# Performance work log

Measured on AMD Instinct MI355X. Metric: run time of the kernel, lower is better.

Reference implementation:

```python
import jax, jax.numpy as jnp
import numpy as np

B, T, I, H, P = 256, 2048, 2, 128, 129  # batch, max_len, input feats, hidden, num_pitches


def setup_inputs() -> dict:
    key = jax.random.key(0)
    ks = jax.random.split(key, 8)
    s = 1.0 / np.sqrt(H)  # torch LSTM/Linear init scale
    x = jax.random.normal(ks[0], (B, T, I), jnp.float32)
    lengths = jax.random.randint(ks[1], (B,), 1, T + 1, jnp.int32)
    W_ih = jax.random.uniform(ks[2], (4 * H, I), jnp.float32, -s, s)
    W_hh = jax.random.uniform(ks[3], (4 * H, H), jnp.float32, -s, s)
    note_W = jax.random.uniform(ks[4], (P, H), jnp.float32, -s, s)
    note_b = jax.random.uniform(ks[5], (P,), jnp.float32, -s, s)
    dur_W = jax.random.uniform(ks[6], (1, H), jnp.float32, -s, s)
    dur_b = jax.random.uniform(ks[7], (1,), jnp.float32, -s, s)
    return dict(x=x, lengths=lengths, W_ih=W_ih, W_hh=W_hh,
                note_W=note_W, note_b=note_b, dur_W=dur_W, dur_b=dur_b)


def _lstm(x, lengths, W_ih, W_hh):
    # Precompute input projections for all timesteps in one GEMM: [T,B,4H]
    pre = jnp.einsum('bti,gi->tbg', x, W_ih)
    h0 = jnp.zeros((x.shape[0], W_hh.shape[1]), x.dtype)
    c0 = h0
    ts = jnp.arange(x.shape[1])

    def step(carry, inp):
        h, c = carry
        px, t = inp
        gates = px + h @ W_hh.T  # [B,4H], torch gate order: i,f,g,o
        i_g, f_g, g_g, o_g = jnp.split(gates, 4, axis=-1)
        i_g = jax.nn.sigmoid(i_g)
        f_g = jax.nn.sigmoid(f_g)
        o_g = jax.nn.sigmoid(o_g)
        g_g = jnp.tanh(g_g)
        c_new = f_g * c + i_g * g_g
        h_new = o_g * jnp.tanh(c_new)
        m = (t < lengths)[:, None]  # packed semantics: freeze past length
        h2 = jnp.where(m, h_new, h)
        c2 = jnp.where(m, c_new, c)
        return (h2, c2), jnp.where(m, h_new, 0.0)

    (hT, cT), hs = jax.lax.scan(step, (h0, c0), (pre, ts))
    return jnp.transpose(hs, (1, 0, 2)), hT, cT  # [B,T,H], final states = states at last valid step


def reference(x, lengths, W_ih, W_hh, note_W, note_b, dur_W, dur_b):
    hs, hT, cT = _lstm(x, lengths, W_ih, W_hh)
    mask = (jnp.arange(x.shape[1])[None, :] < lengths[:, None])[..., None]
    note_logits = jnp.where(mask, hs @ note_W.T + note_b, 0.0)     # [B,T,129]
    duration_pred = jnp.where(mask, hs @ dur_W.T + dur_b, 0.0)     # [B,T,1]
    return note_logits, duration_pred, hT, cT
```

## Files before the change

kernel.cpp:

```cpp
#include <hip/hip_runtime.h>


typedef _Float16 f16;
typedef _Float16 f16x2 __attribute__((ext_vector_type(2)));
typedef _Float16 f16x8 __attribute__((ext_vector_type(8)));
typedef float    f32x4 __attribute__((ext_vector_type(4)));

#define B_  256
#define T_  2048
#define H_  128
#define P_  129

static constexpr size_t NOTE_N   = (size_t)B_ * T_ * P_;
static constexpr size_t DUR_BASE = NOTE_N;
static constexpr size_t HT_BASE  = DUR_BASE + (size_t)B_ * T_;
static constexpr size_t CT_BASE  = HT_BASE + (size_t)B_ * H_;

#if defined(__has_builtin)
#if __has_builtin(__builtin_amdgcn_fdot2)
#define HAVE_FDOT2 1
#endif
#if __has_builtin(__builtin_amdgcn_exp2f)
#define EXP2F(x) __builtin_amdgcn_exp2f(x)
#endif
#endif
#ifndef EXP2F
#define EXP2F(x) __expf((x) * 0.6931471805599453f)
#endif

__device__ __forceinline__ float dot2_acc(f16x2 a, f16x2 b, float c) {
#ifdef HAVE_FDOT2
    return __builtin_amdgcn_fdot2(a, b, c, false);
#else
    return c + (float)a[0] * (float)b[0] + (float)a[1] * (float)b[1];
#endif
}

__device__ __forceinline__ float fast_rcp(float x) { return __builtin_amdgcn_rcpf(x); }

__device__ __forceinline__ float sigmoid_f(float x) {
    float e = EXP2F(-1.44269504f * x);
    return fast_rcp(1.f + e);
}
__device__ __forceinline__ float tanh_f(float x) {
    float e = EXP2F(2.885390082f * x);
    return (e - 1.f) * fast_rcp(e + 1.f);
}

__device__ __forceinline__ float pair_allsum(float v) {
    int a = __float_as_int(v);
    v += __int_as_float(__builtin_amdgcn_mov_dpp(a, 0xB1, 0xF, 0xF, true));
    return v;
}

__device__ __forceinline__ f16* hs_row(float* out, int bt) {
    size_t byteoff = ((size_t)bt * (P_ * 4) + 15) & ~(size_t)15;
    return (f16*)((char*)out + byteoff);
}

__global__ __launch_bounds__(256) void prep_k(const float* __restrict__ note_W,
                                              const float* __restrict__ dur_W,
                                              f16* __restrict__ Wn) {
    int i = threadIdx.x + blockIdx.x * 256;
    if (i >= 144 * 128) return;
    int row = i >> 7, k = i & 127;
    float v = 0.f;
    if (row < 129)       v = note_W[row * 128 + k];
    else if (row == 129) v = dur_W[k];
    Wn[i] = (f16)v;
}

__global__ __launch_bounds__(256, 1) void lstm6_k(const float* __restrict__ x,
                                                  const int* __restrict__ lengths,
                                                  const float* __restrict__ W_ih,
                                                  const float* __restrict__ W_hh,
                                                  float* __restrict__ out) {
    __shared__ __align__(16) f16 h_sh[2][H_];
    __shared__ __align__(8) float2 xs[128];

    const int tid = threadIdx.x;
    const int b = blockIdx.x;
    const int j  = tid >> 1;
    const int kh = tid & 1;
    const bool writer = (kh == 0);

    union WU { f16x8 v8[32]; f16x2 v2[128]; } wu;
    float wix[4], wiy[4];
#pragma unroll
    for (int g = 0; g < 4; g++) {
        const int c = j + 128 * g;
        const float* wr = W_hh + (size_t)c * H_ + 64 * kh;
#pragma unroll
        for (int i = 0; i < 8; i++) {
            float4 v1 = *(const float4*)(wr + 8 * i);
            float4 v2 = *(const float4*)(wr + 8 * i + 4);
            f16x8 f;
            f[0] = (f16)v1.x; f[1] = (f16)v1.y; f[2] = (f16)v1.z; f[3] = (f16)v1.w;
            f[4] = (f16)v2.x; f[5] = (f16)v2.y; f[6] = (f16)v2.z; f[7] = (f16)v2.w;
            wu.v8[8 * g + i] = f;
        }
        wix[g] = W_ih[2 * c];
        wiy[g] = W_ih[2 * c + 1];
    }
    const int len = lengths[b];
    ((f16*)h_sh)[tid] = (f16)0.f;

    char* hp = (char*)out + (size_t)b * (T_ * 516ULL) + 2 * j;

    float c_reg = 0.f, h_reg = 0.f;

    for (int t = 0; t < len; t++) {
        if ((t & 127) == 0) {
            __syncthreads();
            if (tid < 128)
                xs[tid] = *(const float2*)(x + (size_t)b * T_ * 2 + (size_t)(t + tid) * 2);
            __syncthreads();
        }
        const int cur = t & 1;

        union HU { f16x8 v8[8]; f16x2 v2[32]; } hu;
#pragma unroll
        for (int i = 0; i < 8; i++)
            hu.v8[i] = *(const f16x8*)(&h_sh[cur][64 * kh + 8 * i]);

        float a0 = 0.f, a1 = 0.f, a2 = 0.f, a3 = 0.f;
        float b0 = 0.f, b1 = 0.f, b2 = 0.f, b3 = 0.f;
#pragma unroll
        for (int i = 0; i < 16; i++) {
            f16x2 hp0 = hu.v2[i];
            f16x2 hq0 = hu.v2[i + 16];
            a0 = dot2_acc(wu.v2[i],       hp0, a0);
            b0 = dot2_acc(wu.v2[i + 16],  hq0, b0);
            a1 = dot2_acc(wu.v2[i + 32],  hp0, a1);
            b1 = dot2_acc(wu.v2[i + 48],  hq0, b1);
            a2 = dot2_acc(wu.v2[i + 64],  hp0, a2);
            b2 = dot2_acc(wu.v2[i + 80],  hq0, b2);
            a3 = dot2_acc(wu.v2[i + 96],  hp0, a3);
            b3 = dot2_acc(wu.v2[i + 112], hq0, b3);
        }
        a0 += b0; a1 += b1; a2 += b2; a3 += b3;
        a0 = pair_allsum(a0);
        a1 = pair_allsum(a1);
        a2 = pair_allsum(a2);
        a3 = pair_allsum(a3);
        const float2 xv = xs[t & 127];
        a0 += __builtin_fmaf(wiy[0], xv.y, wix[0] * xv.x);
        a1 += __builtin_fmaf(wiy[1], xv.y, wix[1] * xv.x);
        a2 += __builtin_fmaf(wiy[2], xv.y, wix[2] * xv.x);
        a3 += __builtin_fmaf(wiy[3], xv.y, wix[3] * xv.x);

        const float ig = sigmoid_f(a0);
        const float fg = sigmoid_f(a1);
        const float gg = tanh_f(a2);
        const float og = sigmoid_f(a3);
        c_reg = __builtin_fmaf(fg, c_reg, ig * gg);
        h_reg = og * tanh_f(fminf(fmaxf(c_reg, -15.f), 15.f));

        if (writer) {
            const f16 h16 = (f16)h_reg;
            *(f16*)hp = h16;
            h_sh[cur ^ 1][j] = h16;
        }
        hp += 512 + (((t & 3) == 0) ? 16 : 0);

        asm volatile("s_waitcnt lgkmcnt(0)" ::: "memory");
        __builtin_amdgcn_sched_barrier(0);
        __builtin_amdgcn_s_barrier();
        __builtin_amdgcn_sched_barrier(0);
    }

    if (writer) {
        out[HT_BASE + (size_t)b * H_ + j] = h_reg;
        out[CT_BASE + (size_t)b * H_ + j] = c_reg;
    }
}

__global__ __launch_bounds__(256) void proj_k(const int* __restrict__ lengths,
                                              const f16* __restrict__ Wn,
                                              const float* __restrict__ note_b,
                                              const float* __restrict__ dur_b,
                                              float* __restrict__ out) {
    __shared__ __align__(16) f16 wn_sh[144 * 136];

    const int tid = threadIdx.x;
    {
        unsigned int* dst = (unsigned int*)wn_sh;
        const unsigned int* src = (const unsigned int*)Wn;
        for (int w = tid; w < 144 * 64; w += 256) {
            int row = w >> 6, cw = w & 63;
            dst[row * 68 + cw] = src[w];
        }
    }
    __syncthreads();

    const int wv = tid >> 6;
    const int l = tid & 63;
    const int tile = blockIdx.x * 4 + wv;
    const int bt0 = tile * 16;
    const int b = bt0 >> 11;
    const int t0 = bt0 & 2047;
    const int len = lengths[b];
    const int r16 = l & 15, q = l >> 4;

    f32x4 acc[9];
#pragma unroll
    for (int nf = 0; nf < 9; nf++) acc[nf] = f32x4{0.f, 0.f, 0.f, 0.f};

    const bool live = (t0 < len);
    if (live) {
        f16x8 a[4];
        {
            const f16* ar = hs_row(out, bt0 + r16);
#pragma unroll
            for (int kk = 0; kk < 4; kk++)
                a[kk] = *(const f16x8*)(ar + kk * 32 + q * 8);
        }
#pragma unroll
        for (int nf = 0; nf < 9; nf++) {
            const f16* brow = wn_sh + (nf * 16 + r16) * 136 + q * 8;
#pragma unroll
            for (int kk = 0; kk < 4; kk++) {
                f16x8 bb = *(const f16x8*)(brow + kk * 32);
                acc[nf] = __builtin_amdgcn_mfma_f32_16x16x32_f16(a[kk], bb, acc[nf], 0, 0, 0);
            }
        }
    }

#pragma unroll
    for (int nf = 0; nf < 9; nf++) {
        int col = nf * 16 + r16;
        float bias = 0.f;
        if (col < 129)       bias = note_b[col];
        else if (col == 129) bias = dur_b[0];
#pragma unroll
        for (int r = 0; r < 4; r++) {
            int rowbt = bt0 + q * 4 + r;
            int t = t0 + q * 4 + r;
            float v = (t < len) ? (acc[nf][r] + bias) : 0.f;
            if (col < 129)
                out[(size_t)rowbt * P_ + col] = v;
            else if (col == 129)
                out[DUR_BASE + rowbt] = v;
        }
    }
}

extern "C" void kernel_launch(void* const* d_in, const int* in_sizes, int n_in,
                              void* d_out, int out_size, void* d_ws, size_t ws_size,
                              hipStream_t stream) {
    const float* x       = (const float*)d_in[0];
    const int*   lengths = (const int*)d_in[1];
    const float* W_ih    = (const float*)d_in[2];
    const float* W_hh    = (const float*)d_in[3];
    const float* note_W  = (const float*)d_in[4];
    const float* note_b  = (const float*)d_in[5];
    const float* dur_W   = (const float*)d_in[6];
    const float* dur_b   = (const float*)d_in[7];
    float* out = (float*)d_out;
    f16* Wn = (f16*)d_ws;

    prep_k<<<72, 256, 0, stream>>>(note_W, dur_W, Wn);
    lstm6_k<<<B_, 256, 0, stream>>>(x, lengths, W_ih, W_hh, out);
    proj_k<<<(B_ * T_) / 64, 256, 0, stream>>>(lengths, Wn, note_b, dur_b, out);
}
```

Baseline: 1.127 ms.

## Pack two batch rows per block, one on MFMA and one on dot2 units

The LSTM kernel now runs two sequences per 512-thread block. The first half computes the recurrent matvec with 16x16x32 f16 MFMA instructions and the second half keeps the dot2 path, so matrix and vector units work at the same time. Both halves share the per-step block barrier and loop to the longer of the two lengths, masking updates past each sequence's own length. This halves the block count to 128 on a device with more CUs, at the cost of lockstep coupling and wasted steps on the shorter sequence. The MFMA path also wastes three quarters of its output lanes.

```diff
diff --git a/kernel.cpp b/kernel.cpp
--- a/kernel.cpp
+++ b/kernel.cpp
@@ -57,6 +57,12 @@
     size_t byteoff = ((size_t)bt * (P_ * 4) + 15) & ~(size_t)15;
     return (f16*)((char*)out + byteoff);
 }
+
+#define STEP_BARRIER()                                         \
+    asm volatile("s_waitcnt lgkmcnt(0)" ::: "memory");         \
+    __builtin_amdgcn_sched_barrier(0);                         \
+    __builtin_amdgcn_s_barrier();                              \
+    __builtin_amdgcn_sched_barrier(0);
 
 __global__ __launch_bounds__(256) void prep_k(const float* __restrict__ note_W,
                                               const float* __restrict__ dur_W,
@@ -70,108 +76,208 @@
     Wn[i] = (f16)v;
 }
 
-__global__ __launch_bounds__(256, 1) void lstm6_k(const float* __restrict__ x,
-                                                  const int* __restrict__ lengths,
-                                                  const float* __restrict__ W_ih,
-                                                  const float* __restrict__ W_hh,
-                                                  float* __restrict__ out) {
-    __shared__ __align__(16) f16 h_sh[2][H_];
-    __shared__ __align__(8) float2 xs[128];
+__global__ __launch_bounds__(512, 2) void lstm10_k(const float* __restrict__ x,
+                                                   const int* __restrict__ lengths,
+                                                   const float* __restrict__ W_ih,
+                                                   const float* __restrict__ W_hh,
+                                                   float* __restrict__ out) {
+    __shared__ __align__(16) f16 h_shA[2][H_];
+    __shared__ __align__(16) f16 h_shB[2][H_];
+    __shared__ __align__(8) float2 xsA[128];
+    __shared__ __align__(8) float2 xsB[128];
 
     const int tid = threadIdx.x;
-    const int b = blockIdx.x;
-    const int j  = tid >> 1;
-    const int kh = tid & 1;
-    const bool writer = (kh == 0);
-
-    union WU { f16x8 v8[32]; f16x2 v2[128]; } wu;
-    float wix[4], wiy[4];
-#pragma unroll
-    for (int g = 0; g < 4; g++) {
-        const int c = j + 128 * g;
-        const float* wr = W_hh + (size_t)c * H_ + 64 * kh;
-#pragma unroll
-        for (int i = 0; i < 8; i++) {
-            float4 v1 = *(const float4*)(wr + 8 * i);
-            float4 v2 = *(const float4*)(wr + 8 * i + 4);
-            f16x8 f;
-            f[0] = (f16)v1.x; f[1] = (f16)v1.y; f[2] = (f16)v1.z; f[3] = (f16)v1.w;
-            f[4] = (f16)v2.x; f[5] = (f16)v2.y; f[6] = (f16)v2.z; f[7] = (f16)v2.w;
-            wu.v8[8 * g + i] = f;
-        }
-        wix[g] = W_ih[2 * c];
-        wiy[g] = W_ih[2 * c + 1];
-    }
-    const int len = lengths[b];
-    ((f16*)h_sh)[tid] = (f16)0.f;
-
-    char* hp = (char*)out + (size_t)b * (T_ * 516ULL) + 2 * j;
-
-    float c_reg = 0.f, h_reg = 0.f;
-
-    for (int t = 0; t < len; t++) {
-        if ((t & 127) == 0) {
-            __syncthreads();
-            if (tid < 128)
-                xs[tid] = *(const float2*)(x + (size_t)b * T_ * 2 + (size_t)(t + tid) * 2);
-            __syncthreads();
-        }
-        const int cur = t & 1;
-
-        union HU { f16x8 v8[8]; f16x2 v2[32]; } hu;
-#pragma unroll
-        for (int i = 0; i < 8; i++)
-            hu.v8[i] = *(const f16x8*)(&h_sh[cur][64 * kh + 8 * i]);
-
-        float a0 = 0.f, a1 = 0.f, a2 = 0.f, a3 = 0.f;
-        float b0 = 0.f, b1 = 0.f, b2 = 0.f, b3 = 0.f;
-#pragma unroll
-        for (int i = 0; i < 16; i++) {
-            f16x2 hp0 = hu.v2[i];
-            f16x2 hq0 = hu.v2[i + 16];
-            a0 = dot2_acc(wu.v2[i],       hp0, a0);
-            b0 = dot2_acc(wu.v2[i + 16],  hq0, b0);
-            a1 = dot2_acc(wu.v2[i + 32],  hp0, a1);
-            b1 = dot2_acc(wu.v2[i + 48],  hq0, b1);
-            a2 = dot2_acc(wu.v2[i + 64],  hp0, a2);
-            b2 = dot2_acc(wu.v2[i + 80],  hq0, b2);
-            a3 = dot2_acc(wu.v2[i + 96],  hp0, a3);
-            b3 = dot2_acc(wu.v2[i + 112], hq0, b3);
-        }
-        a0 += b0; a1 += b1; a2 += b2; a3 += b3;
-        a0 = pair_allsum(a0);
-        a1 = pair_allsum(a1);
-        a2 = pair_allsum(a2);
-        a3 = pair_allsum(a3);
-        const float2 xv = xs[t & 127];
-        a0 += __builtin_fmaf(wiy[0], xv.y, wix[0] * xv.x);
-        a1 += __builtin_fmaf(wiy[1], xv.y, wix[1] * xv.x);
-        a2 += __builtin_fmaf(wiy[2], xv.y, wix[2] * xv.x);
-        a3 += __builtin_fmaf(wiy[3], xv.y, wix[3] * xv.x);
-
-        const float ig = sigmoid_f(a0);
-        const float fg = sigmoid_f(a1);
-        const float gg = tanh_f(a2);
-        const float og = sigmoid_f(a3);
-        c_reg = __builtin_fmaf(fg, c_reg, ig * gg);
-        h_reg = og * tanh_f(fminf(fmaxf(c_reg, -15.f), 15.f));
+    const int g = blockIdx.x;
+    const int bA = 2 * g, bB = 2 * g + 1;
+    const int lenA = lengths[bA], lenB = lengths[bB];
+    const int maxlen = max(lenA, lenB);
+
+    if (tid < 256) ((f16*)h_shA)[tid] = (f16)0.f;
+    else           ((f16*)h_shB)[tid - 256] = (f16)0.f;
+
+    if (tid < 256) {
+        const int w = tid >> 6, l = tid & 63;
+        const int p = l & 15, q = l >> 4;
+        const int sel = q >> 1;
+        const int j = 16 * w + 64 * sel + p;
+        const bool writer = ((q & 1) == 0);
+
+        f16x8 Bf[8][4];
+        float wxx[8], wxy[8];
+#pragma unroll
+        for (int s = 0; s < 8; s++) {
+            const int c = 16 * (w + 4 * s) + p;
+            const float* wr = W_hh + (size_t)c * H_ + 8 * q;
+#pragma unroll
+            for (int kt = 0; kt < 4; kt++) {
+                float4 v1 = *(const float4*)(wr + 32 * kt);
+                float4 v2 = *(const float4*)(wr + 32 * kt + 4);
+                f16x8 f;
+                f[0]=(f16)v1.x; f[1]=(f16)v1.y; f[2]=(f16)v1.z; f[3]=(f16)v1.w;
+                f[4]=(f16)v2.x; f[5]=(f16)v2.y; f[6]=(f16)v2.z; f[7]=(f16)v2.w;
+                Bf[s][kt] = f;
+            }
+            wxx[s] = W_ih[2 * c];
+            wxy[s] = W_ih[2 * c + 1];
+        }
+
+        char* hp = (char*)out + (size_t)bA * (T_ * 516ULL) + 2 * j;
+        const f32x4 z4 = {0.f, 0.f, 0.f, 0.f};
+        float c_reg = 0.f, h_reg = 0.f;
+
+        for (int t = 0; t < maxlen; t++) {
+            if ((t & 127) == 0) {
+                __syncthreads();
+                if (tid < 128)
+                    xsA[tid] = *(const float2*)(x + (size_t)bA * T_ * 2 + (size_t)(t + tid) * 2);
+                __syncthreads();
+            }
+            const int cur = t & 1;
+
+            f16x8 Af[4];
+#pragma unroll
+            for (int kt = 0; kt < 4; kt++)
+                Af[kt] = *(const f16x8*)(&h_shA[cur][32 * kt + 8 * q]);
+
+            f32x4 acc[8];
+#pragma unroll
+            for (int s = 0; s < 8; s++)
+                acc[s] = __builtin_amdgcn_mfma_f32_16x16x32_f16(Af[0], Bf[s][0], z4, 0, 0, 0);
+#pragma unroll
+            for (int kt = 1; kt < 4; kt++) {
+#pragma unroll
+                for (int s = 0; s < 8; s++)
+                    acc[s] = __builtin_amdgcn_mfma_f32_16x16x32_f16(
+                        Af[kt], Bf[s][kt], acc[s], 0, 0, 0);
+            }
+
+            const float2 xv = xsA[t & 127];
+            float G[4];
+#pragma unroll
+            for (int tt = 0; tt < 4; tt++) {
+                float ga = acc[2 * tt][0] +
+                           __builtin_fmaf(wxy[2 * tt], xv.y, wxx[2 * tt] * xv.x);
+                float gb = acc[2 * tt + 1][0] +
+                           __builtin_fmaf(wxy[2 * tt + 1], xv.y, wxx[2 * tt + 1] * xv.x);
+                G[tt] = sel ? gb : ga;
+            }
+
+            const float ig = sigmoid_f(G[0]);
+            const float fg = sigmoid_f(G[1]);
+            const float gg = tanh_f(G[2]);
+            const float og = sigmoid_f(G[3]);
+            float cn = __builtin_fmaf(fg, c_reg, ig * gg);
+            float hn = og * tanh_f(fminf(fmaxf(cn, -15.f), 15.f));
+            const bool m = (t < lenA);
+            c_reg = m ? cn : c_reg;
+            h_reg = m ? hn : h_reg;
+
+            if (writer) {
+                const f16 h16 = (f16)h_reg;
+                if (m) *(f16*)hp = h16;
+                h_shA[cur ^ 1][j] = h16;
+            }
+            hp += 512 + (((t & 3) == 0) ? 16 : 0);
+
+            STEP_BARRIER();
+        }
 
         if (writer) {
-            const f16 h16 = (f16)h_reg;
-            *(f16*)hp = h16;
-            h_sh[cur ^ 1][j] = h16;
-        }
-        hp += 512 + (((t & 3) == 0) ? 16 : 0);
-
-        asm volatile("s_waitcnt lgkmcnt(0)" ::: "memory");
-        __builtin_amdgcn_sched_barrier(0);
-        __builtin_amdgcn_s_barrier();
-        __builtin_amdgcn_sched_barrier(0);
-    }
-
-    if (writer) {
-        out[HT_BASE + (size_t)b * H_ + j] = h_reg;
-        out[CT_BASE + (size_t)b * H_ + j] = c_reg;
+            out[HT_BASE + (size_t)bA * H_ + j] = h_reg;
+            out[CT_BASE + (size_t)bA * H_ + j] = c_reg;
+        }
+    } else {
+        const int ltid = tid - 256;
+        const int j = ltid >> 1;
+        const int kh = ltid & 1;
+        const bool writer = (kh == 0);
+
+        union WU { f16x8 v8[32]; f16x2 v2[128]; } wu;
+        float wix[4], wiy[4];
+#pragma unroll
+        for (int gg_ = 0; gg_ < 4; gg_++) {
+            const int c = j + 128 * gg_;
+            const float* wr = W_hh + (size_t)c * H_ + 64 * kh;
+#pragma unroll
+            for (int i = 0; i < 8; i++) {
+                float4 v1 = *(const float4*)(wr + 8 * i);
+                float4 v2 = *(const float4*)(wr + 8 * i + 4);
+                f16x8 f;
+                f[0]=(f16)v1.x; f[1]=(f16)v1.y; f[2]=(f16)v1.z; f[3]=(f16)v1.w;
+                f[4]=(f16)v2.x; f[5]=(f16)v2.y; f[6]=(f16)v2.z; f[7]=(f16)v2.w;
+                wu.v8[8 * gg_ + i] = f;
+            }
+            wix[gg_] = W_ih[2 * c];
+            wiy[gg_] = W_ih[2 * c + 1];
+        }
+
+        char* hp = (char*)out + (size_t)bB * (T_ * 516ULL) + 2 * j;
+        float c_reg = 0.f, h_reg = 0.f;
+
+        for (int t = 0; t < maxlen; t++) {
+            if ((t & 127) == 0) {
+                __syncthreads();
+                if (ltid < 128)
+                    xsB[ltid] = *(const float2*)(x + (size_t)bB * T_ * 2 + (size_t)(t + ltid) * 2);
+                __syncthreads();
+            }
+            const int cur = t & 1;
+
+            union HU { f16x8 v8[8]; f16x2 v2[32]; } hu;
+#pragma unroll
+            for (int i = 0; i < 8; i++)
+                hu.v8[i] = *(const f16x8*)(&h_shB[cur][64 * kh + 8 * i]);
+
+            float a0 = 0.f, a1 = 0.f, a2 = 0.f, a3 = 0.f;
+            float b0 = 0.f, b1 = 0.f, b2 = 0.f, b3 = 0.f;
+#pragma unroll
+            for (int i = 0; i < 16; i++) {
+                f16x2 hp0 = hu.v2[i];
+                f16x2 hq0 = hu.v2[i + 16];
+                a0 = dot2_acc(wu.v2[i],       hp0, a0);
+                b0 = dot2_acc(wu.v2[i + 16],  hq0, b0);
+                a1 = dot2_acc(wu.v2[i + 32],  hp0, a1);
+                b1 = dot2_acc(wu.v2[i + 48],  hq0, b1);
+                a2 = dot2_acc(wu.v2[i + 64],  hp0, a2);
+                b2 = dot2_acc(wu.v2[i + 80],  hq0, b2);
+                a3 = dot2_acc(wu.v2[i + 96],  hp0, a3);
+                b3 = dot2_acc(wu.v2[i + 112], hq0, b3);
+            }
+            a0 += b0; a1 += b1; a2 += b2; a3 += b3;
+            a0 = pair_allsum(a0);
+            a1 = pair_allsum(a1);
+            a2 = pair_allsum(a2);
+            a3 = pair_allsum(a3);
+            const float2 xv = xsB[t & 127];
+            a0 += __builtin_fmaf(wiy[0], xv.y, wix[0] * xv.x);
+            a1 += __builtin_fmaf(wiy[1], xv.y, wix[1] * xv.x);
+            a2 += __builtin_fmaf(wiy[2], xv.y, wix[2] * xv.x);
+            a3 += __builtin_fmaf(wiy[3], xv.y, wix[3] * xv.x);
+
+            const float ig = sigmoid_f(a0);
+            const float fg = sigmoid_f(a1);
+            const float gg = tanh_f(a2);
+            const float og = sigmoid_f(a3);
+            float cn = __builtin_fmaf(fg, c_reg, ig * gg);
+            float hn = og * tanh_f(fminf(fmaxf(cn, -15.f), 15.f));
+            const bool m = (t < lenB);
+            c_reg = m ? cn : c_reg;
+            h_reg = m ? hn : h_reg;
+
+            if (writer) {
+                const f16 h16 = (f16)h_reg;
+                if (m) *(f16*)hp = h16;
+                h_shB[cur ^ 1][j] = h16;
+            }
+            hp += 512 + (((t & 3) == 0) ? 16 : 0);
+
+            STEP_BARRIER();
+        }
+
+        if (writer) {
+            out[HT_BASE + (size_t)bB * H_ + j] = h_reg;
+            out[CT_BASE + (size_t)bB * H_ + j] = c_reg;
+        }
     }
 }
 
@@ -260,6 +366,6 @@
     f16* Wn = (f16*)d_ws;
 
     prep_k<<<72, 256, 0, stream>>>(note_W, dur_W, Wn);
-    lstm6_k<<<B_, 256, 0, stream>>>(x, lengths, W_ih, W_hh, out);
+    lstm10_k<<<B_ / 2, 512, 0, stream>>>(x, lengths, W_ih, W_hh, out);
     proj_k<<<(B_ * T_) / 64, 256, 0, stream>>>(lengths, Wn, note_b, dur_b, out);
 }
```

After: 1.798 ms. +59.5%, slower.
